# Performance work log

Hardware: AMD Instinct MI355X
Metric: run time of the kernel (lower is better)

The kernel has to match this reference:

```python
import jax, jax.numpy as jnp
import numpy as np


def setup_inputs() -> dict:
    key = jax.random.key(0)
    ks = jax.random.split(key, 5)
    B, S, D, E, H = 8, 4096, 512, 4, 64
    x = jax.random.normal(ks[0], (B, S, D), dtype=jnp.float32)
    router_w = jax.random.normal(ks[1], (D, E), dtype=jnp.float32) * 0.02
    router_b = jnp.zeros((E,), dtype=jnp.float32)
    w1 = jax.random.normal(ks[2], (E, D, H), dtype=jnp.float32) * 0.02
    b1 = jnp.zeros((E, H), dtype=jnp.float32)
    w2 = jax.random.normal(ks[3], (E, H, D), dtype=jnp.float32) * 0.02
    b2 = jnp.zeros((E, D), dtype=jnp.float32)
    return {"x": x, "router_w": router_w, "router_b": router_b,
            "w1": w1, "b1": b1, "w2": w2, "b2": b2}


def reference(x, router_w, router_b, w1, b1, w2, b2):
    # Router: softmax over experts. weights: [B, S, E]
    weights = jax.nn.softmax(jnp.einsum('bsd,de->bse', x, router_w) + router_b, axis=-1)
    # All experts run densely on every token (batched over the E axis).
    # h: [B, S, E, H]; TF Dense(activation='gelu') uses exact (non-tanh) gelu.
    h = jax.nn.gelu(jnp.einsum('bsd,edh->bseh', x, w1) + b1, approximate=False)
    # expert outputs: [B, S, E, D]; Dropout is identity at inference.
    expert_out = jnp.einsum('bseh,ehd->bsed', h, w2) + b2
    # weighted sum over experts -> [B, S, D]
    return jnp.sum(expert_out * weights[..., None], axis=2)
```

## Files before the change

kernel.cpp:

```cpp
#include <hip/hip_runtime.h>
#include <hip/hip_bf16.h>
#include <math.h>


typedef short v8s __attribute__((ext_vector_type(8)));
typedef float v4f __attribute__((ext_vector_type(4)));

#define XS 520
#define HS 296

__device__ __forceinline__ unsigned short f2bf(float f) {
    unsigned int u = __builtin_bit_cast(unsigned int, f);
    u += 0x7fffu + ((u >> 16) & 1u);
    return (unsigned short)(u >> 16);
}

__global__ void moe_prep(const float* __restrict__ w1,
                         const float* __restrict__ w2,
                         const float* __restrict__ b2,
                         const float* __restrict__ rw,
                         unsigned short* __restrict__ w1p,
                         unsigned short* __restrict__ w2p,
                         unsigned short* __restrict__ rp) {
    int idx = blockIdx.x * 256 + threadIdx.x;
    if (idx < 131072) {
        int block = idx >> 9, within = idx & 511;
        int kb = block >> 4, cb = block & 15;
        int n = within >> 5, kl = within & 31;
        int k = kb * 32 + kl;
        int col = cb * 16 + n;
        int e = col >> 6, h = col & 63;
        w1p[idx] = f2bf(w1[(e * 512 + k) * 64 + h]);
    } else if (idx < 131072 + 147456) {
        int op = idx - 131072;
        int block = op >> 9, within = op & 511;
        int kb = block >> 5, cb = block & 31;
        int n = within >> 5, kl = within & 31;
        int k = kb * 32 + kl;
        int d = cb * 16 + n;
        float v = 0.f;
        if (k < 256) {
            int e = k >> 6, h = k & 63;
            v = w2[(e * 64 + h) * 512 + d];
        } else if (k < 260) {
            v = b2[(k - 256) * 512 + d];
        }
        w2p[op] = f2bf(v);
    } else if (idx < 131072 + 147456 + 8192) {
        int op = idx - (131072 + 147456);
        int kb = op >> 9, within = op & 511;
        int n = within >> 5, kl = within & 31;
        int k = kb * 32 + kl;
        float v = (n < 4) ? rw[k * 4 + n] : 0.f;
        rp[op] = f2bf(v);
    }
}

__global__ __launch_bounds__(256, 2)
void moe_main(const float* __restrict__ x,
              const float* __restrict__ rb,
              const float* __restrict__ b1,
              const unsigned short* __restrict__ w1p,
              const unsigned short* __restrict__ w2p,
              const unsigned short* __restrict__ rp,
              float* __restrict__ out) {
    __shared__ __align__(16) unsigned short lx[64 * XS];
    __shared__ float llog[64 * 4];
    __shared__ float lw[64 * 4];

    const int tid  = threadIdx.x;
    const int lane = tid & 63, wv = tid >> 6;
    const int lr = lane & 15, lq = lane >> 4;
    const long t0 = (long)blockIdx.x * 64;

    const float4* xt = (const float4*)(x + t0 * 512);
    #pragma unroll
    for (int it = 0; it < 32; ++it) {
        int F = it * 256 + tid;
        int row = F >> 7, c4 = F & 127;
        float4 v = xt[F];
        unsigned int p0 = (unsigned int)f2bf(v.x) | ((unsigned int)f2bf(v.y) << 16);
        unsigned int p1 = (unsigned int)f2bf(v.z) | ((unsigned int)f2bf(v.w) << 16);
        *(uint2*)&lx[row * XS + c4 * 4] = make_uint2(p0, p1);
    }
    __syncthreads();

    {
        v4f accR; accR[0] = accR[1] = accR[2] = accR[3] = 0.f;
        #pragma unroll
        for (int kb = 0; kb < 16; ++kb) {
            v8s a = *(const v8s*)(const void*)&lx[(16 * wv + lr) * XS + kb * 32 + lq * 8];
            v8s b = *(const v8s*)(const void*)&rp[kb * 512 + lr * 32 + lq * 8];
            accR = __builtin_amdgcn_mfma_f32_16x16x32_bf16(a, b, accR, 0, 0, 0);
        }
        if (lr < 4) {
            #pragma unroll
            for (int r = 0; r < 4; ++r)
                llog[(16 * wv + lq * 4 + r) * 4 + lr] = accR[r];
        }
    }
    __syncthreads();
    if (tid < 64) {
        float l[4];
        #pragma unroll
        for (int e = 0; e < 4; ++e) l[e] = llog[tid * 4 + e] + rb[e];
        float mx = fmaxf(fmaxf(l[0], l[1]), fmaxf(l[2], l[3]));
        float ex[4], s = 0.f;
        #pragma unroll
        for (int e = 0; e < 4; ++e) { ex[e] = expf(l[e] - mx); s += ex[e]; }
        float inv = 1.f / s;
        #pragma unroll
        for (int e = 0; e < 4; ++e) lw[tid * 4 + e] = ex[e] * inv;
    }
    __syncthreads();

    v4f acc1[4][4];
    #pragma unroll
    for (int mt = 0; mt < 4; ++mt)
        #pragma unroll
        for (int nt = 0; nt < 4; ++nt)
            acc1[mt][nt][0] = acc1[mt][nt][1] = acc1[mt][nt][2] = acc1[mt][nt][3] = 0.f;

    for (int kb = 0; kb < 16; ++kb) {
        v8s a[4], b[4];
        #pragma unroll
        for (int mt = 0; mt < 4; ++mt)
            a[mt] = *(const v8s*)(const void*)&lx[(16 * mt + lr) * XS + kb * 32 + lq * 8];
        #pragma unroll
        for (int nt = 0; nt < 4; ++nt)
            b[nt] = *(const v8s*)(const void*)&w1p[(size_t)(kb * 16 + wv * 4 + nt) * 512 + lr * 32 + lq * 8];
        #pragma unroll
        for (int mt = 0; mt < 4; ++mt)
            #pragma unroll
            for (int nt = 0; nt < 4; ++nt)
                acc1[mt][nt] = __builtin_amdgcn_mfma_f32_16x16x32_bf16(a[mt], b[nt], acc1[mt][nt], 0, 0, 0);
    }
    __syncthreads();

    {
        float b1v[4];
        #pragma unroll
        for (int nt = 0; nt < 4; ++nt) b1v[nt] = b1[wv * 64 + nt * 16 + lr];
        #pragma unroll
        for (int mt = 0; mt < 4; ++mt) {
            #pragma unroll
            for (int r = 0; r < 4; ++r) {
                int row = 16 * mt + lq * 4 + r;
                float wt = lw[row * 4 + wv];
                #pragma unroll
                for (int nt = 0; nt < 4; ++nt) {
                    float v = acc1[mt][nt][r] + b1v[nt];
                    float g = 0.5f * v * (1.f + erff(v * 0.70710678118f)) * wt;
                    lx[row * HS + wv * 64 + nt * 16 + lr] = f2bf(g);
                }
            }
        }
        int r = tid >> 2, e = tid & 3;
        lx[r * HS + 256 + e] = f2bf(lw[tid]);
        #pragma unroll
        for (int i = 0; i < 7; ++i)
            lx[r * HS + 260 + e + 4 * i] = 0;
    }
    __syncthreads();

    v4f acc2[4][8];
    #pragma unroll
    for (int mt = 0; mt < 4; ++mt)
        #pragma unroll
        for (int nt = 0; nt < 8; ++nt)
            acc2[mt][nt][0] = acc2[mt][nt][1] = acc2[mt][nt][2] = acc2[mt][nt][3] = 0.f;

    for (int kb = 0; kb < 9; ++kb) {
        v8s a[4], b[8];
        #pragma unroll
        for (int mt = 0; mt < 4; ++mt)
            a[mt] = *(const v8s*)(const void*)&lx[(16 * mt + lr) * HS + kb * 32 + lq * 8];
        #pragma unroll
        for (int nt = 0; nt < 8; ++nt)
            b[nt] = *(const v8s*)(const void*)&w2p[(size_t)(kb * 32 + wv * 8 + nt) * 512 + lr * 32 + lq * 8];
        #pragma unroll
        for (int mt = 0; mt < 4; ++mt)
            #pragma unroll
            for (int nt = 0; nt < 8; ++nt)
                acc2[mt][nt] = __builtin_amdgcn_mfma_f32_16x16x32_bf16(a[mt], b[nt], acc2[mt][nt], 0, 0, 0);
    }

    float* ot = out + t0 * 512;
    #pragma unroll
    for (int mt = 0; mt < 4; ++mt)
        #pragma unroll
        for (int nt = 0; nt < 8; ++nt)
            #pragma unroll
            for (int r = 0; r < 4; ++r) {
                int row = 16 * mt + lq * 4 + r;
                int col = 128 * wv + 16 * nt + lr;
                ot[row * 512 + col] = acc2[mt][nt][r];
            }
}

extern "C" void kernel_launch(void* const* d_in, const int* in_sizes, int n_in,
                              void* d_out, int out_size, void* d_ws, size_t ws_size,
                              hipStream_t stream) {
    const float* x  = (const float*)d_in[0];
    const float* rw = (const float*)d_in[1];
    const float* rb = (const float*)d_in[2];
    const float* w1 = (const float*)d_in[3];
    const float* b1 = (const float*)d_in[4];
    const float* w2 = (const float*)d_in[5];
    const float* b2 = (const float*)d_in[6];

    unsigned short* w1p = (unsigned short*)d_ws;
    unsigned short* w2p = w1p + 131072;
    unsigned short* rp  = w2p + 147456;

    moe_prep<<<1120, 256, 0, stream>>>(w1, w2, b2, rw, w1p, w2p, rp);
    moe_main<<<512, 256, 0, stream>>>(x, rb, b1, w1p, w2p, rp, (float*)d_out);
}
```

Baseline: 142.4 us.

## Give each wave its own 16-token tile and drop block-level barriers

Each wave now handles an independent 16-token slice: it converts its own x rows, computes router softmax, the first GEMM over all 256 hidden columns, and the second GEMM over all 512 outputs in two passes. The change removes every __syncthreads and uses only per-wave lgkmcnt waits, so waves no longer stall on each other. The cost is weight reuse: each wave streams the whole w1p and w2p from global/L2 for just 16 rows, where before B fragments were shared across 64 rows. This raises weight traffic per token about fourfold and lowers MFMA work per B load.

```diff
diff --git a/kernel.cpp b/kernel.cpp
--- a/kernel.cpp
+++ b/kernel.cpp
@@ -64,138 +64,125 @@
               const unsigned short* __restrict__ w2p,
               const unsigned short* __restrict__ rp,
               float* __restrict__ out) {
-    __shared__ __align__(16) unsigned short lx[64 * XS];
-    __shared__ float llog[64 * 4];
-    __shared__ float lw[64 * 4];
+    __shared__ __align__(16) unsigned short lx[4 * 16 * XS];
+    __shared__ float llog[4 * 16 * 4];
+    __shared__ float lw[4 * 16 * 4];
 
     const int tid  = threadIdx.x;
     const int lane = tid & 63, wv = tid >> 6;
     const int lr = lane & 15, lq = lane >> 4;
-    const long t0 = (long)blockIdx.x * 64;
+    const long t0 = (long)blockIdx.x * 64 + wv * 16;
+
+    unsigned short* W  = lx + wv * 16 * XS;
+    float* wlog = llog + wv * 64;
+    float* wlw  = lw   + wv * 64;
 
     const float4* xt = (const float4*)(x + t0 * 512);
     #pragma unroll
     for (int it = 0; it < 32; ++it) {
-        int F = it * 256 + tid;
+        int F = it * 64 + lane;
         int row = F >> 7, c4 = F & 127;
         float4 v = xt[F];
         unsigned int p0 = (unsigned int)f2bf(v.x) | ((unsigned int)f2bf(v.y) << 16);
         unsigned int p1 = (unsigned int)f2bf(v.z) | ((unsigned int)f2bf(v.w) << 16);
-        *(uint2*)&lx[row * XS + c4 * 4] = make_uint2(p0, p1);
-    }
-    __syncthreads();
+        *(uint2*)&W[row * XS + c4 * 4] = make_uint2(p0, p1);
+    }
 
     {
         v4f accR; accR[0] = accR[1] = accR[2] = accR[3] = 0.f;
         #pragma unroll
         for (int kb = 0; kb < 16; ++kb) {
-            v8s a = *(const v8s*)(const void*)&lx[(16 * wv + lr) * XS + kb * 32 + lq * 8];
+            v8s a = *(const v8s*)(const void*)&W[lr * XS + kb * 32 + lq * 8];
             v8s b = *(const v8s*)(const void*)&rp[kb * 512 + lr * 32 + lq * 8];
             accR = __builtin_amdgcn_mfma_f32_16x16x32_bf16(a, b, accR, 0, 0, 0);
         }
         if (lr < 4) {
             #pragma unroll
             for (int r = 0; r < 4; ++r)
-                llog[(16 * wv + lq * 4 + r) * 4 + lr] = accR[r];
-        }
-    }
-    __syncthreads();
-    if (tid < 64) {
-        float l[4];
-        #pragma unroll
-        for (int e = 0; e < 4; ++e) l[e] = llog[tid * 4 + e] + rb[e];
-        float mx = fmaxf(fmaxf(l[0], l[1]), fmaxf(l[2], l[3]));
-        float ex[4], s = 0.f;
-        #pragma unroll
-        for (int e = 0; e < 4; ++e) { ex[e] = expf(l[e] - mx); s += ex[e]; }
-        float inv = 1.f / s;
-        #pragma unroll
-        for (int e = 0; e < 4; ++e) lw[tid * 4 + e] = ex[e] * inv;
-    }
-    __syncthreads();
-
-    v4f acc1[4][4];
+                wlog[(lq * 4 + r) * 4 + lr] = accR[r];
+        }
+        asm volatile("s_waitcnt lgkmcnt(0)" ::: "memory");
+        if (lane < 16) {
+            float l[4];
+            #pragma unroll
+            for (int e = 0; e < 4; ++e) l[e] = wlog[lane * 4 + e] + rb[e];
+            float mx = fmaxf(fmaxf(l[0], l[1]), fmaxf(l[2], l[3]));
+            float ex[4], s = 0.f;
+            #pragma unroll
+            for (int e = 0; e < 4; ++e) { ex[e] = expf(l[e] - mx); s += ex[e]; }
+            float inv = 1.f / s;
+            #pragma unroll
+            for (int e = 0; e < 4; ++e) wlw[lane * 4 + e] = ex[e] * inv;
+        }
+        asm volatile("s_waitcnt lgkmcnt(0)" ::: "memory");
+    }
+
+    v4f acc1[16];
     #pragma unroll
-    for (int mt = 0; mt < 4; ++mt)
-        #pragma unroll
-        for (int nt = 0; nt < 4; ++nt)
-            acc1[mt][nt][0] = acc1[mt][nt][1] = acc1[mt][nt][2] = acc1[mt][nt][3] = 0.f;
+    for (int nt = 0; nt < 16; ++nt)
+        acc1[nt][0] = acc1[nt][1] = acc1[nt][2] = acc1[nt][3] = 0.f;
 
     for (int kb = 0; kb < 16; ++kb) {
-        v8s a[4], b[4];
-        #pragma unroll
-        for (int mt = 0; mt < 4; ++mt)
-            a[mt] = *(const v8s*)(const void*)&lx[(16 * mt + lr) * XS + kb * 32 + lq * 8];
-        #pragma unroll
-        for (int nt = 0; nt < 4; ++nt)
-            b[nt] = *(const v8s*)(const void*)&w1p[(size_t)(kb * 16 + wv * 4 + nt) * 512 + lr * 32 + lq * 8];
-        #pragma unroll
-        for (int mt = 0; mt < 4; ++mt)
-            #pragma unroll
-            for (int nt = 0; nt < 4; ++nt)
-                acc1[mt][nt] = __builtin_amdgcn_mfma_f32_16x16x32_bf16(a[mt], b[nt], acc1[mt][nt], 0, 0, 0);
-    }
-    __syncthreads();
+        v8s a = *(const v8s*)(const void*)&W[lr * XS + kb * 32 + lq * 8];
+        #pragma unroll
+        for (int nt = 0; nt < 16; ++nt) {
+            v8s b = *(const v8s*)(const void*)&w1p[(size_t)(kb * 16 + nt) * 512 + lr * 32 + lq * 8];
+            acc1[nt] = __builtin_amdgcn_mfma_f32_16x16x32_bf16(a, b, acc1[nt], 0, 0, 0);
+        }
+    }
+    asm volatile("s_waitcnt lgkmcnt(0)" ::: "memory");
 
     {
-        float b1v[4];
-        #pragma unroll
-        for (int nt = 0; nt < 4; ++nt) b1v[nt] = b1[wv * 64 + nt * 16 + lr];
-        #pragma unroll
-        for (int mt = 0; mt < 4; ++mt) {
+        #pragma unroll
+        for (int nt = 0; nt < 16; ++nt) {
+            float bb = b1[nt * 16 + lr];
+            float wt4[4];
+            #pragma unroll
+            for (int r = 0; r < 4; ++r) wt4[r] = wlw[(lq * 4 + r) * 4 + (nt >> 2)];
             #pragma unroll
             for (int r = 0; r < 4; ++r) {
-                int row = 16 * mt + lq * 4 + r;
-                float wt = lw[row * 4 + wv];
-                #pragma unroll
-                for (int nt = 0; nt < 4; ++nt) {
-                    float v = acc1[mt][nt][r] + b1v[nt];
-                    float g = 0.5f * v * (1.f + erff(v * 0.70710678118f)) * wt;
-                    lx[row * HS + wv * 64 + nt * 16 + lr] = f2bf(g);
-                }
+                int row = lq * 4 + r;
+                float v = acc1[nt][r] + bb;
+                float g = 0.5f * v * (1.f + erff(v * 0.70710678118f)) * wt4[r];
+                W[row * HS + nt * 16 + lr] = f2bf(g);
             }
         }
-        int r = tid >> 2, e = tid & 3;
-        lx[r * HS + 256 + e] = f2bf(lw[tid]);
-        #pragma unroll
-        for (int i = 0; i < 7; ++i)
-            lx[r * HS + 260 + e + 4 * i] = 0;
-    }
-    __syncthreads();
-
-    v4f acc2[4][8];
-    #pragma unroll
-    for (int mt = 0; mt < 4; ++mt)
-        #pragma unroll
-        for (int nt = 0; nt < 8; ++nt)
-            acc2[mt][nt][0] = acc2[mt][nt][1] = acc2[mt][nt][2] = acc2[mt][nt][3] = 0.f;
-
-    for (int kb = 0; kb < 9; ++kb) {
-        v8s a[4], b[8];
-        #pragma unroll
-        for (int mt = 0; mt < 4; ++mt)
-            a[mt] = *(const v8s*)(const void*)&lx[(16 * mt + lr) * HS + kb * 32 + lq * 8];
-        #pragma unroll
-        for (int nt = 0; nt < 8; ++nt)
-            b[nt] = *(const v8s*)(const void*)&w2p[(size_t)(kb * 32 + wv * 8 + nt) * 512 + lr * 32 + lq * 8];
-        #pragma unroll
-        for (int mt = 0; mt < 4; ++mt)
-            #pragma unroll
-            for (int nt = 0; nt < 8; ++nt)
-                acc2[mt][nt] = __builtin_amdgcn_mfma_f32_16x16x32_bf16(a[mt], b[nt], acc2[mt][nt], 0, 0, 0);
-    }
+        #pragma unroll
+        for (int i = 0; i < 8; ++i) {
+            int idx = i * 64 + lane;
+            int row = idx >> 5, c = idx & 31;
+            unsigned short v = (c < 4) ? f2bf(wlw[row * 4 + c]) : (unsigned short)0;
+            W[row * HS + 256 + c] = v;
+        }
+    }
+    asm volatile("s_waitcnt lgkmcnt(0)" ::: "memory");
 
     float* ot = out + t0 * 512;
     #pragma unroll
-    for (int mt = 0; mt < 4; ++mt)
-        #pragma unroll
-        for (int nt = 0; nt < 8; ++nt)
+    for (int np = 0; np < 2; ++np) {
+        v4f acc2[16];
+        #pragma unroll
+        for (int nt = 0; nt < 16; ++nt)
+            acc2[nt][0] = acc2[nt][1] = acc2[nt][2] = acc2[nt][3] = 0.f;
+
+        for (int kb = 0; kb < 9; ++kb) {
+            v8s a = *(const v8s*)(const void*)&W[lr * HS + kb * 32 + lq * 8];
+            #pragma unroll
+            for (int nt = 0; nt < 16; ++nt) {
+                v8s b = *(const v8s*)(const void*)&w2p[(size_t)(kb * 32 + np * 16 + nt) * 512 + lr * 32 + lq * 8];
+                acc2[nt] = __builtin_amdgcn_mfma_f32_16x16x32_bf16(a, b, acc2[nt], 0, 0, 0);
+            }
+        }
+
+        #pragma unroll
+        for (int nt = 0; nt < 16; ++nt)
             #pragma unroll
             for (int r = 0; r < 4; ++r) {
-                int row = 16 * mt + lq * 4 + r;
-                int col = 128 * wv + 16 * nt + lr;
-                ot[row * 512 + col] = acc2[mt][nt][r];
+                int row = lq * 4 + r;
+                int col = np * 256 + nt * 16 + lr;
+                ot[row * 512 + col] = acc2[nt][r];
             }
+    }
 }
 
 extern "C" void kernel_launch(void* const* d_in, const int* in_sizes, int n_in,
```

New measurement: 187.6 us. 1.32x slower.
